# Kernel tuning notes

Hardware: AMD Instinct MI355X
Metric: run time of the kernel (lower is better)

The kernel has to match this reference:

```python
import jax, jax.numpy as jnp
from jax import lax
import numpy as np

N_HEAD = 16
KERNEL = 3
ROPE_BASE = 10000.0


def _rope_tables(T, D, dtype):
    inv_freq = 1.0 / (ROPE_BASE ** (jnp.arange(0, D, 2, dtype=jnp.float32) / D))
    t = jnp.arange(T, dtype=jnp.float32)
    freqs = t[:, None] * inv_freq[None, :]           # [T, D/2]
    emb = jnp.concatenate([freqs, freqs], axis=-1)   # [T, D]
    return jnp.cos(emb).astype(dtype), jnp.sin(emb).astype(dtype)


def _rotate_half(x):
    x1, x2 = jnp.split(x, 2, axis=-1)
    return jnp.concatenate([-x2, x1], axis=-1)


def setup_inputs() -> dict:
    key = jax.random.key(0)
    k1, k2, k3, k4 = jax.random.split(key, 4)
    B, T, C = 2, 2048, 2048
    s = 0.02
    return {
        "x": jax.random.normal(k1, (B, T, C), dtype=jnp.float32),
        "conv_w": jax.random.normal(k2, (C, 1, KERNEL), dtype=jnp.float32) * s,
        "w_attn": jax.random.normal(k3, (3 * C, C), dtype=jnp.float32) * s,
        "w_proj": jax.random.normal(k4, (C, C), dtype=jnp.float32) * s,
    }


def reference(x, conv_w, w_attn, w_proj):
    B, T, C = x.shape
    H = N_HEAD
    D = C // H

    # causal depthwise conv1d: left-pad K-1, groups=C
    xc = jnp.transpose(x, (0, 2, 1))                       # [B, C, T]
    xc = jnp.pad(xc, ((0, 0), (0, 0), (KERNEL - 1, 0)))
    xc = lax.conv_general_dilated(
        xc, conv_w, window_strides=(1,), padding="VALID",
        feature_group_count=C, dimension_numbers=("NCH", "OIH", "NCH"))
    xconv = jnp.transpose(xc, (0, 2, 1))                   # [B, T, C]

    # fused QKV projection
    qkv = xconv @ w_attn.T                                 # [B, T, 3C]
    q, k, v = jnp.split(qkv, 3, axis=-1)
    q = q.reshape(B, T, H, D)
    k = k.reshape(B, T, H, D)
    v = v.reshape(B, T, H, D)

    # rotary embedding
    cos, sin = _rope_tables(T, D, x.dtype)                 # [T, D]
    cos = cos[None, :, None, :]
    sin = sin[None, :, None, :]
    q = q * cos + _rotate_half(q) * sin
    k = k * cos + _rotate_half(k) * sin

    # causal SDPA
    scale = 1.0 / jnp.sqrt(jnp.asarray(D, dtype=x.dtype))
    scores = jnp.einsum("bthd,bshd->bhts", q, k) * scale   # [B, H, T, T]
    causal = jnp.tril(jnp.ones((T, T), dtype=bool))
    scores = jnp.where(causal[None, None], scores, jnp.finfo(scores.dtype).min)
    p = jax.nn.softmax(scores, axis=-1)
    y = jnp.einsum("bhts,bshd->bthd", p, v).reshape(B, T, C)

    return y @ w_proj.T
```

## Files before the change

### kernel.cpp

```cpp
#include <hip/hip_runtime.h>

typedef __attribute__((ext_vector_type(8))) short bf16x8;
typedef __attribute__((ext_vector_type(4))) float f32x4;
typedef __attribute__((ext_vector_type(4))) unsigned short u16x4;

#define DEV static __device__ __forceinline__

DEV float bf2f(unsigned short u) {
  union { unsigned int i; float f; } v; v.i = ((unsigned int)u) << 16; return v.f;
}
DEV unsigned short f2bf(float f) {
  unsigned int x = __float_as_uint(f);
  x += 0x7fffu + ((x >> 16) & 1u);
  return (unsigned short)(x >> 16);
}
DEV f32x4 mfma16(bf16x8 a, bf16x8 b, f32x4 c) {
  return __builtin_amdgcn_mfma_f32_16x16x32_bf16(a, b, c, 0, 0, 0);
}
DEV void gload_lds16(const void* g, void* l) {
  __builtin_amdgcn_global_load_lds(
      (const __attribute__((address_space(1))) unsigned int*)g,
      (__attribute__((address_space(3))) unsigned int*)l, 16, 0, 0);
}

__global__ void build_tables(float* __restrict__ ct, float* __restrict__ st) {
  int idx = blockIdx.x * 256 + threadIdx.x;
  int i = idx & 63, t = idx >> 6;
  float f = powf(10000.0f, -(float)i * (1.0f / 64.0f));
  float a = (float)t * f;
  ct[idx] = cosf(a);
  st[idx] = sinf(a);
}

__global__ void cast_bf(const float* __restrict__ in, unsigned short* __restrict__ out, int n4) {
  int idx = blockIdx.x * 256 + threadIdx.x;
  if (idx >= n4) return;
  f32x4 v = *(const f32x4*)(in + (size_t)idx * 4);
  u16x4 o;
  #pragma unroll
  for (int j = 0; j < 4; ++j) o[j] = f2bf(v[j]);
  *(u16x4*)(out + (size_t)idx * 4) = o;
}

__global__ void conv_cast(const float* __restrict__ x, const float* __restrict__ w,
                          unsigned short* __restrict__ out) {
  int idx = blockIdx.x * 256 + threadIdx.x;
  int c4 = idx & 511, t = (idx >> 9) & 2047;
  int c = c4 * 4;
  const float* xp = x + (size_t)(idx >> 20) * 2048 * 2048 + (size_t)t * 2048 + c;
  f32x4 v2 = *(const f32x4*)xp;
  f32x4 v1 = {0.f, 0.f, 0.f, 0.f}, v0 = {0.f, 0.f, 0.f, 0.f};
  if (t >= 1) v1 = *(const f32x4*)(xp - 2048);
  if (t >= 2) v0 = *(const f32x4*)(xp - 4096);
  u16x4 o;
  #pragma unroll
  for (int j = 0; j < 4; ++j) {
    float val = v0[j] * w[(c + j) * 3 + 0] + v1[j] * w[(c + j) * 3 + 1] + v2[j] * w[(c + j) * 3 + 2];
    o[j] = f2bf(val);
  }
  *(u16x4*)(idx * 4 + out) = o;
}

template <int NFRAG, bool OUT_BF16>
__global__ __launch_bounds__(512, 2) void gemm8(const unsigned short* __restrict__ A,
                                                const unsigned short* __restrict__ Bw,
                                                void* __restrict__ Cp, int M, int N, int K) {
  constexpr int BN = NFRAG * 64;
  constexpr int BLD = (NFRAG >= 4) ? 2 : 1;
  __shared__ __align__(16) unsigned short As[2][2][256 * 32];
  __shared__ __align__(16) unsigned short Bs[2][2][BN * 32];
  const int tid = threadIdx.x;
  const int w = tid >> 6, l = tid & 63;
  const int lr = l & 15, lg = l >> 4;
  const int wm = w >> 2, wn = w & 3;
  const int nbx = N / BN, nby = M >> 8;
  const int nwg = nbx * nby;
  const int bid = blockIdx.x;
  const int wg = (bid & 7) * (nwg >> 3) + (bid >> 3);
  const int bx = wg / nby, by = wg % nby;
  const int m0 = by << 8, n0 = bx * BN;

  int aOff[2], bOff[2];
  #pragma unroll
  for (int it = 0; it < 2; ++it) {
    int q = it * 512 + tid, row = q >> 2, cp = q & 3;
    aOff[it] = (m0 + row) * K + ((cp ^ ((row >> 1) & 3)) * 8);
  }
  #pragma unroll
  for (int it = 0; it < BLD; ++it) {
    int q = it * 512 + tid, row = q >> 2, cp = q & 3;
    bOff[it] = (n0 + row) * K + ((cp ^ ((row >> 1) & 3)) * 8);
  }
  const int dstW = w * 64 * 8;

  int aRd[8], bRd[NFRAG];
  #pragma unroll
  for (int m = 0; m < 8; ++m) {
    int R = wm * 128 + m * 16 + lr;
    aRd[m] = R * 32 + ((lg ^ ((R >> 1) & 3)) * 8);
  }
  #pragma unroll
  for (int n = 0; n < NFRAG; ++n) {
    int R = wn * (NFRAG * 16) + n * 16 + lr;
    bRd[n] = R * 32 + ((lg ^ ((R >> 1) & 3)) * 8);
  }

  auto stageA = [&](int tt, int kh) {
    const unsigned short* s = A + (size_t)(tt * 64 + kh * 32);
    unsigned short* d = (unsigned short*)As[tt & 1][kh] + dstW;
    gload_lds16(s + aOff[0], d);
    gload_lds16(s + aOff[1], d + 4096);
  };
  auto stageB = [&](int tt, int kh) {
    const unsigned short* s = Bw + (size_t)(tt * 64 + kh * 32);
    unsigned short* d = (unsigned short*)Bs[tt & 1][kh] + dstW;
    gload_lds16(s + bOff[0], d);
    if constexpr (BLD == 2) gload_lds16(s + bOff[1], d + 4096);
  };
  #define WAIT_STEADY()                                            \
    if constexpr (NFRAG == 4) asm volatile("s_waitcnt vmcnt(4)" ::: "memory"); \
    else                      asm volatile("s_waitcnt vmcnt(3)" ::: "memory")

  f32x4 acc[8][NFRAG] = {};
  const int NT = K >> 6;
  stageA(0, 0); stageB(0, 0); stageA(0, 1); stageB(0, 1);
  stageA(1, 0); stageB(1, 0);
  __builtin_amdgcn_sched_barrier(0);
  WAIT_STEADY();
  __builtin_amdgcn_s_barrier();
  __builtin_amdgcn_sched_barrier(0);

  #define PHASE(KH, MH, STAGE_STMT, WAIT_STMT)                                  \
  {                                                                             \
    const unsigned short* Ab = (const unsigned short*)As[t & 1][KH];            \
    const unsigned short* Bb = (const unsigned short*)Bs[t & 1][KH];            \
    bf16x8 aF[4], bF[NFRAG];                                                    \
    _Pragma("unroll") for (int j = 0; j < 4; ++j)                               \
        aF[j] = *(const bf16x8*)(Ab + aRd[MH * 4 + j]);                         \
    _Pragma("unroll") for (int n = 0; n < NFRAG; ++n)                           \
        bF[n] = *(const bf16x8*)(Bb + bRd[n]);                                  \
    STAGE_STMT;                                                                 \
    __builtin_amdgcn_sched_barrier(0);                                          \
    __builtin_amdgcn_s_barrier();                                               \
    __builtin_amdgcn_sched_barrier(0);                                          \
    __builtin_amdgcn_s_setprio(1);                                              \
    _Pragma("unroll") for (int j = 0; j < 4; ++j)                               \
      _Pragma("unroll") for (int n = 0; n < NFRAG; ++n)                         \
          acc[MH * 4 + j][n] = mfma16(aF[j], bF[n], acc[MH * 4 + j][n]);        \
    __builtin_amdgcn_s_setprio(0);                                              \
    WAIT_STMT;                                                                  \
    __builtin_amdgcn_sched_barrier(0);                                          \
    __builtin_amdgcn_s_barrier();                                               \
    __builtin_amdgcn_sched_barrier(0);                                          \
  }

  for (int t = 0; t < NT; ++t) {
    PHASE(0, 0, { if (t + 1 < NT) stageA(t + 1, 1); }, {});
    PHASE(0, 1, { if (t + 1 < NT) stageB(t + 1, 1); }, {});
    PHASE(1, 0, { if (t + 2 < NT) stageA(t + 2, 0); }, {});
    PHASE(1, 1, { if (t + 2 < NT) stageB(t + 2, 0); },
          { if (t + 2 < NT) { WAIT_STEADY(); }
            else asm volatile("s_waitcnt vmcnt(0)" ::: "memory"); });
  }
  #undef PHASE
  #undef WAIT_STEADY

  #pragma unroll
  for (int m = 0; m < 8; ++m)
    #pragma unroll
    for (int r = 0; r < 4; ++r) {
      int row = m0 + wm * 128 + m * 16 + lg * 4 + r;
      #pragma unroll
      for (int n = 0; n < NFRAG; ++n) {
        int col = n0 + wn * (NFRAG * 16) + n * 16 + lr;
        if (OUT_BF16) ((unsigned short*)Cp)[(size_t)row * N + col] = f2bf(acc[m][n][r]);
        else          ((float*)Cp)[(size_t)row * N + col] = acc[m][n][r];
      }
    }
}

__global__ void rope_repack(const unsigned short* __restrict__ qkv, const float* __restrict__ ct,
                            const float* __restrict__ st, unsigned short* __restrict__ Qo,
                            unsigned short* __restrict__ Ko) {
  int idx = blockIdx.x * 256 + threadIdx.x;
  int i = idx & 63;
  int h = (idx >> 6) & 15;
  int t = (idx >> 10) & 2047;
  int b = idx >> 21;
  const unsigned short* src = qkv + ((size_t)(b * 2048 + t)) * 6144 + h * 128;
  float cz = ct[t * 64 + i], sz = st[t * 64 + i];
  float q1 = bf2f(src[i]),        q2 = bf2f(src[i + 64]);
  float k1 = bf2f(src[2048 + i]), k2 = bf2f(src[2048 + i + 64]);
  size_t o = ((size_t)(b * 16 + h) * 2048 + t) * 128 + i;
  Qo[o]      = f2bf(q1 * cz - q2 * sz);
  Qo[o + 64] = f2bf(q2 * cz + q1 * sz);
  Ko[o]      = f2bf(k1 * cz - k2 * sz);
  Ko[o + 64] = f2bf(k2 * cz + k1 * sz);
}

__global__ __launch_bounds__(256) void v_transpose(const unsigned short* __restrict__ qkv,
                                                   unsigned short* __restrict__ Vt) {
  __shared__ unsigned short tile[64][72];
  const int bh = blockIdx.x;
  const int tt = blockIdx.y;
  const int dd = blockIdx.z;
  const int b = bh >> 4, h = bh & 15;
  const unsigned short* src = qkv + ((size_t)(b * 2048 + tt * 64)) * 6144 + 4096 + h * 128 + dd * 64;
  const int row = threadIdx.x >> 2;
  const int ch = threadIdx.x & 3;
  #pragma unroll
  for (int it = 0; it < 2; ++it) {
    int d0 = (ch * 2 + it) * 8;
    *(bf16x8*)&tile[row][d0] = *(const bf16x8*)(src + (size_t)row * 6144 + d0);
  }
  __syncthreads();
  unsigned short* dst = Vt + ((size_t)bh * 128 + dd * 64) * 2048 + tt * 64;
  #pragma unroll
  for (int it = 0; it < 2; ++it) {
    int t0 = (ch * 2 + it) * 8;
    bf16x8 v;
    #pragma unroll
    for (int j = 0; j < 8; ++j) ((unsigned short*)&v)[j] = tile[t0 + j][row];
    *(bf16x8*)(dst + (size_t)row * 2048 + t0) = v;
  }
}

__global__ __launch_bounds__(256, 4) void attn_fwd(const unsigned short* __restrict__ Q,
                                                   const unsigned short* __restrict__ K,
                                                   const unsigned short* __restrict__ Vt,
                                                   unsigned short* __restrict__ Y) {
  const int T = 2048, D = 128, C = 2048;
  __shared__ __align__(16) unsigned short Ks[64 * 128];
  __shared__ __align__(16) unsigned short Vs[128 * 64];
  __shared__ __align__(16) unsigned short Pl[4][16 * 64];
  const int tid = threadIdx.x;
  const int w = tid >> 6, l = tid & 63;
  const int lr = l & 15, lg = l >> 4;
  const int bh = blockIdx.x;
  const int qi = (int)gridDim.y - 1 - (int)blockIdx.y;
  const int qbase = qi * 64;
  const size_t base = (size_t)bh * T * D;

  bf16x8 qf[4];
  {
    const unsigned short* qp = Q + base + (size_t)(qbase + w * 16 + lr) * D + lg * 8;
    #pragma unroll
    for (int d = 0; d < 4; ++d) qf[d] = *(const bf16x8*)(qp + d * 32);
  }
  int kSrc[4], vSrc[4], ldsDst[4];
  #pragma unroll
  for (int it = 0; it < 4; ++it) {
    int c = it * 256 + tid;
    int krow = c >> 4, kdc = c & 15;
    kSrc[it] = krow * D + ((kdc ^ (krow & 7)) * 8);
    int vd = c >> 3, vcc = c & 7;
    vSrc[it] = vd * T + ((vcc ^ (vd & 7)) * 8);
    ldsDst[it] = (it * 256 + w * 64) * 8;
  }
  f32x4 ao[8] = {};
  float mrun = -3.0e38f, lrun = 0.0f;
  const float cs = 0.08838834764831845f * 1.4426950408889634f;
  const int q_abs = qbase + w * 16 + lr;

  for (int kt = 0; kt <= qi; ++kt) {
    const int kv0 = kt * 64;
    #pragma unroll
    for (int it = 0; it < 4; ++it) {
      gload_lds16(K + base + (size_t)kv0 * D + kSrc[it], Ks + ldsDst[it]);
      gload_lds16(Vt + base + kv0 + vSrc[it], Vs + ldsDst[it]);
    }
    __syncthreads();
    f32x4 s4[4] = {};
    __builtin_amdgcn_s_setprio(1);
    #pragma unroll
    for (int n = 0; n < 4; ++n) {
      int row = n * 16 + lr;
      #pragma unroll
      for (int d = 0; d < 4; ++d) {
        bf16x8 kf = *(const bf16x8*)(Ks + row * 128 + (((d * 4 + lg) ^ (lr & 7)) * 8));
        s4[n] = mfma16(kf, qf[d], s4[n]);
      }
    }
    __builtin_amdgcn_s_setprio(0);
    if (kt == qi) {
      #pragma unroll
      for (int n = 0; n < 4; ++n)
        #pragma unroll
        for (int r = 0; r < 4; ++r)
          if (kv0 + n * 16 + lg * 4 + r > q_abs) s4[n][r] = -3.0e38f;
    }
    float mx = -3.0e38f;
    #pragma unroll
    for (int n = 0; n < 4; ++n)
      #pragma unroll
      for (int r = 0; r < 4; ++r) mx = fmaxf(mx, s4[n][r]);
    mx = fmaxf(mx, __shfl_xor(mx, 16, 64));
    mx = fmaxf(mx, __shfl_xor(mx, 32, 64));
    float mnew = fmaxf(mrun, mx);
    float fac = exp2f((mrun - mnew) * cs);
    mrun = mnew;
    float sum = 0.0f;
    #pragma unroll
    for (int n = 0; n < 4; ++n)
      #pragma unroll
      for (int r = 0; r < 4; ++r) {
        float p = exp2f((s4[n][r] - mnew) * cs);
        s4[n][r] = p;
        sum += p;
      }
    sum += __shfl_xor(sum, 16, 64);
    sum += __shfl_xor(sum, 32, 64);
    lrun = lrun * fac + sum;
    float fr[4];
    #pragma unroll
    for (int r = 0; r < 4; ++r) fr[r] = __shfl(fac, (l & 48) | (lg * 4 + r), 64);
    #pragma unroll
    for (int n8 = 0; n8 < 8; ++n8)
      #pragma unroll
      for (int r = 0; r < 4; ++r) ao[n8][r] *= fr[r];
    unsigned short* pw = (unsigned short*)Pl[w];
    #pragma unroll
    for (int n = 0; n < 4; ++n)
      #pragma unroll
      for (int i = 0; i < 2; ++i) {
        unsigned int pk = (unsigned int)f2bf(s4[n][2 * i]) |
                          ((unsigned int)f2bf(s4[n][2 * i + 1]) << 16);
        int kv = n * 16 + lg * 4 + 2 * i;
        *(unsigned int*)(pw + lr * 64 + (((kv >> 3) ^ (lr & 7)) * 8) + (kv & 7)) = pk;
      }
    __builtin_amdgcn_s_setprio(1);
    #pragma unroll
    for (int ks = 0; ks < 2; ++ks) {
      bf16x8 pa = *(const bf16x8*)(pw + lr * 64 + (((ks * 4 + lg) ^ (lr & 7)) * 8));
      #pragma unroll
      for (int n = 0; n < 8; ++n) {
        int row = n * 16 + lr;
        bf16x8 vb = *(const bf16x8*)(Vs + row * 64 + (((ks * 4 + lg) ^ (lr & 7)) * 8));
        ao[n] = mfma16(pa, vb, ao[n]);
      }
    }
    __builtin_amdgcn_s_setprio(0);
    __syncthreads();
  }
  const int b = bh >> 4, h = bh & 15;
  #pragma unroll
  for (int r = 0; r < 4; ++r) {
    float lsum = __shfl(lrun, (l & 48) | (lg * 4 + r), 64);
    float inv = 1.0f / lsum;
    int t = qbase + w * 16 + lg * 4 + r;
    unsigned short* dst = Y + ((size_t)b * T + t) * C + h * D;
    #pragma unroll
    for (int n = 0; n < 8; ++n) dst[n * 16 + lr] = f2bf(ao[n][r] * inv);
  }
}

extern "C" void kernel_launch(void* const* d_in, const int* in_sizes, int n_in,
                              void* d_out, int out_size, void* d_ws, size_t ws_size,
                              hipStream_t stream) {
  const float* x      = (const float*)d_in[0];
  const float* conv_w = (const float*)d_in[1];
  const float* w_attn = (const float*)d_in[2];
  const float* w_proj = (const float*)d_in[3];
  float* out = (float*)d_out;
  char* ws = (char*)d_ws;

  unsigned short* qkv  = (unsigned short*)(ws);
  unsigned short* qb   = (unsigned short*)(ws + 50331648);
  unsigned short* kb   = (unsigned short*)(ws + 67108864);
  unsigned short* vt   = (unsigned short*)(ws + 83886080);
  unsigned short* xcy  = (unsigned short*)(ws + 100663296);
  unsigned short* wbuf = (unsigned short*)(ws + 117440512);
  float* ctab = (float*)(ws + 142606336);
  float* stab = (float*)(ws + 143130624);

  build_tables<<<512, 256, 0, stream>>>(ctab, stab);
  cast_bf<<<12288, 256, 0, stream>>>(w_attn, wbuf, 3145728);
  conv_cast<<<8192, 256, 0, stream>>>(x, conv_w, xcy);
  gemm8<4, true><<<384, 512, 0, stream>>>(xcy, wbuf, (void*)qkv, 4096, 6144, 2048);
  rope_repack<<<16384, 256, 0, stream>>>(qkv, ctab, stab, qb, kb);
  v_transpose<<<dim3(32, 32, 2), 256, 0, stream>>>(qkv, vt);
  cast_bf<<<4096, 256, 0, stream>>>(w_proj, wbuf, 1048576);
  attn_fwd<<<dim3(32, 32), 256, 0, stream>>>(qb, kb, vt, xcy);
  gemm8<2, false><<<256, 512, 0, stream>>>(xcy, wbuf, (void*)out, 4096, 2048, 2048);
}
```

Before: 318.6 us.

## Restructure GEMM pipeline into two phases per K-tile and retile output projection

Replaces the four-phase-per-tile GEMM loop, which staged A and B in separate phases, with a two-phase loop. Each phase stages both A and B for a future half-tile and computes all fragments, with explicit prologue/epilogue iterations instead of per-phase conditionals. The output projection GEMM switches from a 256x128 tile to a 128x256 tile. The goal is fewer barriers per K-step and better load/compute overlap, at the cost of different vmcnt wait depths and register pressure per phase (acc stays at 8x4 for QKV).

```diff
diff --git a/kernel.cpp b/kernel.cpp
--- a/kernel.cpp
+++ b/kernel.cpp
@@ -61,28 +61,32 @@
   *(u16x4*)(idx * 4 + out) = o;
 }
 
-template <int NFRAG, bool OUT_BF16>
-__global__ __launch_bounds__(512, 2) void gemm8(const unsigned short* __restrict__ A,
-                                                const unsigned short* __restrict__ Bw,
-                                                void* __restrict__ Cp, int M, int N, int K) {
+template <int MFRAG, int NFRAG, bool OUT_BF16>
+__global__ __launch_bounds__(512, 2) void gemm2p(const unsigned short* __restrict__ A,
+                                                 const unsigned short* __restrict__ Bw,
+                                                 void* __restrict__ Cp, int M, int N, int K) {
+  constexpr int BM = MFRAG * 32;
   constexpr int BN = NFRAG * 64;
-  constexpr int BLD = (NFRAG >= 4) ? 2 : 1;
-  __shared__ __align__(16) unsigned short As[2][2][256 * 32];
+  constexpr int ALD = BM / 128;
+  constexpr int BLD = BN / 128;
+  constexpr int STEADY = 2 * (ALD + BLD);
+  constexpr int HALF = ALD + BLD;
+  __shared__ __align__(16) unsigned short As[2][2][BM * 32];
   __shared__ __align__(16) unsigned short Bs[2][2][BN * 32];
   const int tid = threadIdx.x;
   const int w = tid >> 6, l = tid & 63;
   const int lr = l & 15, lg = l >> 4;
   const int wm = w >> 2, wn = w & 3;
-  const int nbx = N / BN, nby = M >> 8;
+  const int nbx = N / BN, nby = M / BM;
   const int nwg = nbx * nby;
   const int bid = blockIdx.x;
   const int wg = (bid & 7) * (nwg >> 3) + (bid >> 3);
   const int bx = wg / nby, by = wg % nby;
-  const int m0 = by << 8, n0 = bx * BN;
-
-  int aOff[2], bOff[2];
-  #pragma unroll
-  for (int it = 0; it < 2; ++it) {
+  const int m0 = by * BM, n0 = bx * BN;
+
+  int aOff[ALD], bOff[BLD];
+  #pragma unroll
+  for (int it = 0; it < ALD; ++it) {
     int q = it * 512 + tid, row = q >> 2, cp = q & 3;
     aOff[it] = (m0 + row) * K + ((cp ^ ((row >> 1) & 3)) * 8);
   }
@@ -91,12 +95,12 @@
     int q = it * 512 + tid, row = q >> 2, cp = q & 3;
     bOff[it] = (n0 + row) * K + ((cp ^ ((row >> 1) & 3)) * 8);
   }
-  const int dstW = w * 64 * 8;
-
-  int aRd[8], bRd[NFRAG];
-  #pragma unroll
-  for (int m = 0; m < 8; ++m) {
-    int R = wm * 128 + m * 16 + lr;
+  const int dstW = w * 512;
+
+  int aRd[MFRAG], bRd[NFRAG];
+  #pragma unroll
+  for (int m = 0; m < MFRAG; ++m) {
+    int R = wm * (MFRAG * 16) + m * 16 + lr;
     aRd[m] = R * 32 + ((lg ^ ((R >> 1) & 3)) * 8);
   }
   #pragma unroll
@@ -108,68 +112,75 @@
   auto stageA = [&](int tt, int kh) {
     const unsigned short* s = A + (size_t)(tt * 64 + kh * 32);
     unsigned short* d = (unsigned short*)As[tt & 1][kh] + dstW;
-    gload_lds16(s + aOff[0], d);
-    gload_lds16(s + aOff[1], d + 4096);
+    #pragma unroll
+    for (int it = 0; it < ALD; ++it) gload_lds16(s + aOff[it], d + it * 4096);
   };
   auto stageB = [&](int tt, int kh) {
     const unsigned short* s = Bw + (size_t)(tt * 64 + kh * 32);
     unsigned short* d = (unsigned short*)Bs[tt & 1][kh] + dstW;
-    gload_lds16(s + bOff[0], d);
-    if constexpr (BLD == 2) gload_lds16(s + bOff[1], d + 4096);
+    #pragma unroll
+    for (int it = 0; it < BLD; ++it) gload_lds16(s + bOff[it], d + it * 4096);
   };
-  #define WAIT_STEADY()                                            \
-    if constexpr (NFRAG == 4) asm volatile("s_waitcnt vmcnt(4)" ::: "memory"); \
-    else                      asm volatile("s_waitcnt vmcnt(3)" ::: "memory")
-
-  f32x4 acc[8][NFRAG] = {};
+  #define WAIT_STEADY do { if constexpr (STEADY == 8) asm volatile("s_waitcnt vmcnt(8)" ::: "memory"); \
+                           else asm volatile("s_waitcnt vmcnt(6)" ::: "memory"); } while (0)
+  #define WAIT_HALF   do { if constexpr (HALF == 4) asm volatile("s_waitcnt vmcnt(4)" ::: "memory"); \
+                           else asm volatile("s_waitcnt vmcnt(3)" ::: "memory"); } while (0)
+  #define WAIT_ZERO   asm volatile("s_waitcnt vmcnt(0)" ::: "memory")
+
+  #define PH(BUF, KH, STAGE_STMT, WAIT_STMT)                              \
+  {                                                                       \
+    const unsigned short* Ab = (const unsigned short*)As[BUF][KH];        \
+    const unsigned short* Bb = (const unsigned short*)Bs[BUF][KH];        \
+    bf16x8 aF[MFRAG], bF[NFRAG];                                          \
+    _Pragma("unroll") for (int m = 0; m < MFRAG; ++m)                     \
+        aF[m] = *(const bf16x8*)(Ab + aRd[m]);                            \
+    _Pragma("unroll") for (int n = 0; n < NFRAG; ++n)                     \
+        bF[n] = *(const bf16x8*)(Bb + bRd[n]);                            \
+    STAGE_STMT;                                                           \
+    __builtin_amdgcn_sched_barrier(0);                                    \
+    __builtin_amdgcn_s_barrier();                                         \
+    __builtin_amdgcn_sched_barrier(0);                                    \
+    __builtin_amdgcn_s_setprio(1);                                        \
+    _Pragma("unroll") for (int m = 0; m < MFRAG; ++m)                     \
+      _Pragma("unroll") for (int n = 0; n < NFRAG; ++n)                   \
+          acc[m][n] = mfma16(aF[m], bF[n], acc[m][n]);                    \
+    __builtin_amdgcn_s_setprio(0);                                        \
+    WAIT_STMT;                                                            \
+    __builtin_amdgcn_sched_barrier(0);                                    \
+    __builtin_amdgcn_s_barrier();                                         \
+    __builtin_amdgcn_sched_barrier(0);                                    \
+  }
+
+  f32x4 acc[MFRAG][NFRAG] = {};
   const int NT = K >> 6;
-  stageA(0, 0); stageB(0, 0); stageA(0, 1); stageB(0, 1);
+  stageA(0, 0); stageB(0, 0);
+  stageA(0, 1); stageB(0, 1);
   stageA(1, 0); stageB(1, 0);
   __builtin_amdgcn_sched_barrier(0);
-  WAIT_STEADY();
+  WAIT_STEADY;
   __builtin_amdgcn_s_barrier();
   __builtin_amdgcn_sched_barrier(0);
 
-  #define PHASE(KH, MH, STAGE_STMT, WAIT_STMT)                                  \
-  {                                                                             \
-    const unsigned short* Ab = (const unsigned short*)As[t & 1][KH];            \
-    const unsigned short* Bb = (const unsigned short*)Bs[t & 1][KH];            \
-    bf16x8 aF[4], bF[NFRAG];                                                    \
-    _Pragma("unroll") for (int j = 0; j < 4; ++j)                               \
-        aF[j] = *(const bf16x8*)(Ab + aRd[MH * 4 + j]);                         \
-    _Pragma("unroll") for (int n = 0; n < NFRAG; ++n)                           \
-        bF[n] = *(const bf16x8*)(Bb + bRd[n]);                                  \
-    STAGE_STMT;                                                                 \
-    __builtin_amdgcn_sched_barrier(0);                                          \
-    __builtin_amdgcn_s_barrier();                                               \
-    __builtin_amdgcn_sched_barrier(0);                                          \
-    __builtin_amdgcn_s_setprio(1);                                              \
-    _Pragma("unroll") for (int j = 0; j < 4; ++j)                               \
-      _Pragma("unroll") for (int n = 0; n < NFRAG; ++n)                         \
-          acc[MH * 4 + j][n] = mfma16(aF[j], bF[n], acc[MH * 4 + j][n]);        \
-    __builtin_amdgcn_s_setprio(0);                                              \
-    WAIT_STMT;                                                                  \
-    __builtin_amdgcn_sched_barrier(0);                                          \
-    __builtin_amdgcn_s_barrier();                                               \
-    __builtin_amdgcn_sched_barrier(0);                                          \
-  }
-
-  for (int t = 0; t < NT; ++t) {
-    PHASE(0, 0, { if (t + 1 < NT) stageA(t + 1, 1); }, {});
-    PHASE(0, 1, { if (t + 1 < NT) stageB(t + 1, 1); }, {});
-    PHASE(1, 0, { if (t + 2 < NT) stageA(t + 2, 0); }, {});
-    PHASE(1, 1, { if (t + 2 < NT) stageB(t + 2, 0); },
-          { if (t + 2 < NT) { WAIT_STEADY(); }
-            else asm volatile("s_waitcnt vmcnt(0)" ::: "memory"); });
-  }
-  #undef PHASE
+  int t = 0;
+  for (; t + 2 < NT; ++t) {
+    PH(t & 1, 0, { stageA(t + 1, 1); stageB(t + 1, 1); }, WAIT_STEADY);
+    PH(t & 1, 1, { stageA(t + 2, 0); stageB(t + 2, 0); }, WAIT_STEADY);
+  }
+  PH(t & 1, 0, { stageA(t + 1, 1); stageB(t + 1, 1); }, WAIT_STEADY);
+  PH(t & 1, 1, {}, WAIT_HALF);
+  ++t;
+  PH(t & 1, 0, {}, WAIT_ZERO);
+  PH(t & 1, 1, {}, {});
+  #undef PH
   #undef WAIT_STEADY
-
-  #pragma unroll
-  for (int m = 0; m < 8; ++m)
+  #undef WAIT_HALF
+  #undef WAIT_ZERO
+
+  #pragma unroll
+  for (int m = 0; m < MFRAG; ++m)
     #pragma unroll
     for (int r = 0; r < 4; ++r) {
-      int row = m0 + wm * 128 + m * 16 + lg * 4 + r;
+      int row = m0 + wm * (MFRAG * 16) + m * 16 + lg * 4 + r;
       #pragma unroll
       for (int n = 0; n < NFRAG; ++n) {
         int col = n0 + wn * (NFRAG * 16) + n * 16 + lr;
@@ -376,10 +387,10 @@
   build_tables<<<512, 256, 0, stream>>>(ctab, stab);
   cast_bf<<<12288, 256, 0, stream>>>(w_attn, wbuf, 3145728);
   conv_cast<<<8192, 256, 0, stream>>>(x, conv_w, xcy);
-  gemm8<4, true><<<384, 512, 0, stream>>>(xcy, wbuf, (void*)qkv, 4096, 6144, 2048);
+  gemm2p<8, 4, true><<<384, 512, 0, stream>>>(xcy, wbuf, (void*)qkv, 4096, 6144, 2048);
   rope_repack<<<16384, 256, 0, stream>>>(qkv, ctab, stab, qb, kb);
   v_transpose<<<dim3(32, 32, 2), 256, 0, stream>>>(qkv, vt);
   cast_bf<<<4096, 256, 0, stream>>>(w_proj, wbuf, 1048576);
   attn_fwd<<<dim3(32, 32), 256, 0, stream>>>(qb, kb, vt, xcy);
-  gemm8<2, false><<<256, 512, 0, stream>>>(xcy, wbuf, (void*)out, 4096, 2048, 2048);
-}
+  gemm2p<4, 4, false><<<256, 512, 0, stream>>>(xcy, wbuf, (void*)out, 4096, 2048, 2048);
+}
```

Measured after the change: 296.0 us. 1.08x faster.
